# Kernel tuning notes

Measured on AMD Instinct MI355X. Metric: run time of the kernel, lower is better.

The kernel has to match this reference:

```python
import jax, jax.numpy as jnp
import numpy as np

B, F, D = 1024, 4096, 32


def setup_inputs() -> dict:
    key = jax.random.key(0)
    k1, k2, k3, k4 = jax.random.split(key, 4)
    data = jax.random.normal(k1, (B, F), dtype=jnp.float32)
    embed = jax.random.uniform(k2, (F, D), dtype=jnp.float32, minval=-0.05, maxval=0.05)
    bias = jax.random.normal(k3, (F, 1), dtype=jnp.float32) * 0.01
    global_bias = jax.random.normal(k4, (1, 1), dtype=jnp.float32) * 0.01
    return {"data": data, "embed": embed, "bias": bias, "global_bias": global_bias}


def reference(data, embed, bias, global_bias):
    # Original TF: scaled = data[:,:,None] * embed[None]; dot = sum_{i,j} scaled_i . scaled_j
    # Full (diagonal-inclusive) sum of the F x F dot matrix equals ||sum_i scaled_i||^2,
    # identical math in O(B*F*D) instead of O(B*F^2*D).
    scaled = data[:, :, None] * embed[None, :, :]      # (B, F, D)
    s = jnp.sum(scaled, axis=1)                        # (B, D)
    dot = jnp.sum(s * s, axis=-1)                      # (B,)
    bias_term = jnp.sum(data * bias[:, 0][None, :], axis=-1)  # (B,)
    pred = jax.nn.sigmoid(global_bias[0, 0] + bias_term + dot)
    return pred
```

## Files before the change

### kernel.cpp

```cpp
#include <hip/hip_runtime.h>
#include <hip/hip_bf16.h>
#include <math.h>


#define F_DIM 4096
#define D_DIM 32
#define B_DIM 1024
#define MT 16
#define KS 32
#define KC 128
#define LDA 136
#define NW 4

typedef __attribute__((ext_vector_type(8))) short short8;
typedef __attribute__((ext_vector_type(4))) float f32x4;

__device__ inline unsigned int pkbf(float a, float b) {
    __hip_bfloat162 h = __float22bfloat162_rn(make_float2(a, b));
    union { __hip_bfloat162 h2; unsigned int u; } c; c.h2 = h;
    return c.u;
}

__global__ __launch_bounds__(256, 6) void fm_mfma(const float* __restrict__ data,
                                                  const float* __restrict__ embed,
                                                  const float* __restrict__ bias,
                                                  float* __restrict__ ws_s,
                                                  float* __restrict__ ws_b)
{
    __shared__ short lA [MT][LDA];
    __shared__ short lBT[D_DIM][LDA];
    __shared__ float redCT[NW][2][16][20];

    const int t  = threadIdx.x;
    const int w  = t >> 6;
    const int l  = t & 63;
    const int mt = blockIdx.x >> 5;
    const int ks = blockIdx.x & 31;
    const int m0 = mt * MT;
    const int kb = ks * KC;

    const int koff = (l & 31) * 4;
    const float4 bv = *(const float4*)(bias + kb + koff);
    float bt2[2];
    #pragma unroll
    for (int it = 0; it < 2; ++it) {
        const int r = w * 2 + (l >> 5) + it * 8;
        const float4 x = *(const float4*)(data + (size_t)(m0 + r) * F_DIM + kb + koff);
        float s = x.x * bv.x;
        s = fmaf(x.y, bv.y, s);
        s = fmaf(x.z, bv.z, s);
        s = fmaf(x.w, bv.w, s);
        bt2[it] = s;
        uint2 pk;
        pk.x = pkbf(x.x, x.y);
        pk.y = pkbf(x.z, x.w);
        *(uint2*)(&lA[r][koff]) = pk;
    }

    {
        const int d2 = (t & 15) * 2;
        const int k8 = (t >> 4) * 8;
        const float* ep = embed + (size_t)(kb + k8) * D_DIM + d2;
        float2 e[8];
        #pragma unroll
        for (int j = 0; j < 8; ++j) e[j] = *(const float2*)(ep + (size_t)j * D_DIM);
        uint4 ux, uy;
        ux.x = pkbf(e[0].x, e[1].x); ux.y = pkbf(e[2].x, e[3].x);
        ux.z = pkbf(e[4].x, e[5].x); ux.w = pkbf(e[6].x, e[7].x);
        uy.x = pkbf(e[0].y, e[1].y); uy.y = pkbf(e[2].y, e[3].y);
        uy.z = pkbf(e[4].y, e[5].y); uy.w = pkbf(e[6].y, e[7].y);
        *(uint4*)(&lBT[d2    ][k8]) = ux;
        *(uint4*)(&lBT[d2 + 1][k8]) = uy;
    }
    __syncthreads();

    const int quad = l >> 4;
    const int mrow = l & 15;
    const int kk   = w * 32 + quad * 8;
    const short8 a  = *(const short8*)(&lA [mrow     ][kk]);
    const short8 b0 = *(const short8*)(&lBT[mrow     ][kk]);
    const short8 b1 = *(const short8*)(&lBT[16 + mrow][kk]);
    const f32x4 z = {0.f, 0.f, 0.f, 0.f};
    f32x4 acc0 = __builtin_amdgcn_mfma_f32_16x16x32_bf16(a, b0, z, 0, 0, 0);
    f32x4 acc1 = __builtin_amdgcn_mfma_f32_16x16x32_bf16(a, b1, z, 0, 0, 0);

    #pragma unroll
    for (int it = 0; it < 2; ++it) {
        float v = bt2[it];
        v += __shfl_xor(v, 1);  v += __shfl_xor(v, 2);  v += __shfl_xor(v, 4);
        v += __shfl_xor(v, 8);  v += __shfl_xor(v, 16);
        if ((l & 31) == 0)
            ws_b[(size_t)(m0 + w * 2 + (l >> 5) + it * 8) * KS + ks] = v;
    }

    *(f32x4*)(&redCT[w][0][mrow][quad * 4]) = acc0;
    *(f32x4*)(&redCT[w][1][mrow][quad * 4]) = acc1;
    __syncthreads();

    #pragma unroll
    for (int h = 0; h < 2; ++h) {
        const int e  = t + h * 256;
        const int nt = e >> 8;
        const int r  = (e >> 4) & 15;
        const int c  = e & 15;
        const float v = redCT[0][nt][c][r] + redCT[1][nt][c][r]
                      + redCT[2][nt][c][r] + redCT[3][nt][c][r];
        ws_s[((size_t)(m0 + r) * KS + ks) * D_DIM + nt * 16 + c] = v;
    }
}

__global__ __launch_bounds__(256, 4) void fm_final(const float* __restrict__ ws_s,
                                                   const float* __restrict__ ws_b,
                                                   const float* __restrict__ gbias,
                                                   float* __restrict__ out)
{
    const int t = threadIdx.x;
    const int w = t >> 6;
    const int l = t & 63;
    const int row = blockIdx.x * 4 + w;

    float4 v = ((const float4*)(ws_s + (size_t)row * KS * D_DIM))[l];
    #pragma unroll
    for (int m = 8; m <= 32; m <<= 1) {
        v.x += __shfl_xor(v.x, m); v.y += __shfl_xor(v.y, m);
        v.z += __shfl_xor(v.z, m); v.w += __shfl_xor(v.w, m);
    }
    float c = 0.f;
    if (l < 8)  c = v.x * v.x + v.y * v.y + v.z * v.z + v.w * v.w;
    if (l < 32) c += ws_b[(size_t)row * KS + l];
    #pragma unroll
    for (int m = 1; m <= 32; m <<= 1) c += __shfl_xor(c, m);
    if (l == 0) {
        const float x = gbias[0] + c;
        out[row] = 1.0f / (1.0f + __expf(-x));
    }
}

extern "C" void kernel_launch(void* const* d_in, const int* in_sizes, int n_in,
                              void* d_out, int out_size, void* d_ws, size_t ws_size,
                              hipStream_t stream) {
    const float* data  = (const float*)d_in[0];
    const float* embed = (const float*)d_in[1];
    const float* bias  = (const float*)d_in[2];
    const float* gb    = (const float*)d_in[3];
    float* out  = (float*)d_out;

    float* ws_s = (float*)d_ws;
    float* ws_b = (float*)d_ws + (size_t)B_DIM * KS * D_DIM;

    dim3 gridA(64 * KS);
    dim3 blockA(256);
    fm_mfma<<<gridA, blockA, 0, stream>>>(data, embed, bias, ws_s, ws_b);

    dim3 gridB(B_DIM / 4);
    dim3 blockB(256);
    fm_final<<<gridB, blockB, 0, stream>>>(ws_s, ws_b, gb, out);
}
```

Measured before the change: 71.49 us.

## Fuse MFMA partial-sum and final reduction into one cooperative kernel

Merges the two kernels into a single cooperative launch that uses a grid-wide sync between the partial-sum stage and the final sigmoid reduction. The K split drops from 32 to 4 chunks of 1024, and 512-thread blocks accumulate four chained MFMAs per wave. This removes one kernel launch and shrinks the workspace partial traffic. The cost is a grid barrier, only 256 blocks of 512 threads (fewer waves in flight to hide global-load latency), and much larger LDS use per block.

```diff
diff --git a/kernel.cpp b/kernel.cpp
--- a/kernel.cpp
+++ b/kernel.cpp
@@ -1,16 +1,19 @@
 #include <hip/hip_runtime.h>
 #include <hip/hip_bf16.h>
+#include <hip/hip_cooperative_groups.h>
 #include <math.h>
+
+namespace cg = cooperative_groups;
 
 
 #define F_DIM 4096
 #define D_DIM 32
 #define B_DIM 1024
 #define MT 16
-#define KS 32
-#define KC 128
-#define LDA 136
-#define NW 4
+#define KS 4
+#define KC 1024
+#define LDA 1032
+#define NTHREADS 512
 
 typedef __attribute__((ext_vector_type(8))) short short8;
 typedef __attribute__((ext_vector_type(4))) float f32x4;
@@ -21,118 +24,115 @@
     return c.u;
 }
 
-__global__ __launch_bounds__(256, 6) void fm_mfma(const float* __restrict__ data,
-                                                  const float* __restrict__ embed,
-                                                  const float* __restrict__ bias,
-                                                  float* __restrict__ ws_s,
-                                                  float* __restrict__ ws_b)
+__global__ __launch_bounds__(NTHREADS, 2) void fm_fused(
+    const float* __restrict__ data, const float* __restrict__ embed,
+    const float* __restrict__ bias, const float* __restrict__ gbias,
+    float* __restrict__ ws_s, float* __restrict__ ws_b,
+    float* __restrict__ out)
 {
     __shared__ short lA [MT][LDA];
     __shared__ short lBT[D_DIM][LDA];
-    __shared__ float redCT[NW][2][16][20];
+    __shared__ float redCT[8][2][16][20];
 
     const int t  = threadIdx.x;
     const int w  = t >> 6;
     const int l  = t & 63;
-    const int mt = blockIdx.x >> 5;
-    const int ks = blockIdx.x & 31;
+    const int mt = blockIdx.x >> 2;
+    const int ks = blockIdx.x & 3;
     const int m0 = mt * MT;
     const int kb = ks * KC;
 
-    const int koff = (l & 31) * 4;
-    const float4 bv = *(const float4*)(bias + kb + koff);
-    float bt2[2];
-    #pragma unroll
-    for (int it = 0; it < 2; ++it) {
-        const int r = w * 2 + (l >> 5) + it * 8;
-        const float4 x = *(const float4*)(data + (size_t)(m0 + r) * F_DIM + kb + koff);
-        float s = x.x * bv.x;
-        s = fmaf(x.y, bv.y, s);
-        s = fmaf(x.z, bv.z, s);
-        s = fmaf(x.w, bv.w, s);
-        bt2[it] = s;
-        uint2 pk;
-        pk.x = pkbf(x.x, x.y);
-        pk.y = pkbf(x.z, x.w);
-        *(uint2*)(&lA[r][koff]) = pk;
+    {
+        const int r  = t >> 5;
+        const int c4 = (t & 31) * 4;
+        const float* dro = data + (size_t)(m0 + r) * F_DIM + kb;
+        const float* bro = bias + kb;
+        float bt = 0.f;
+        #pragma unroll
+        for (int jj = 0; jj < 8; ++jj) {
+            const int col = c4 + jj * 128;
+            const float4 x  = *(const float4*)(dro + col);
+            const float4 bv = *(const float4*)(bro + col);
+            bt = fmaf(x.x, bv.x, bt);
+            bt = fmaf(x.y, bv.y, bt);
+            bt = fmaf(x.z, bv.z, bt);
+            bt = fmaf(x.w, bv.w, bt);
+            uint2 pk;
+            pk.x = pkbf(x.x, x.y);
+            pk.y = pkbf(x.z, x.w);
+            *(uint2*)(&lA[r][col]) = pk;
+        }
+        bt += __shfl_xor(bt, 1);  bt += __shfl_xor(bt, 2);
+        bt += __shfl_xor(bt, 4);  bt += __shfl_xor(bt, 8);
+        bt += __shfl_xor(bt, 16);
+        if ((t & 31) == 0) ws_b[(size_t)(m0 + r) * KS + ks] = bt;
     }
 
     {
         const int d2 = (t & 15) * 2;
-        const int k8 = (t >> 4) * 8;
-        const float* ep = embed + (size_t)(kb + k8) * D_DIM + d2;
-        float2 e[8];
+        const int kq = t >> 4;
         #pragma unroll
-        for (int j = 0; j < 8; ++j) e[j] = *(const float2*)(ep + (size_t)j * D_DIM);
-        uint4 ux, uy;
-        ux.x = pkbf(e[0].x, e[1].x); ux.y = pkbf(e[2].x, e[3].x);
-        ux.z = pkbf(e[4].x, e[5].x); ux.w = pkbf(e[6].x, e[7].x);
-        uy.x = pkbf(e[0].y, e[1].y); uy.y = pkbf(e[2].y, e[3].y);
-        uy.z = pkbf(e[4].y, e[5].y); uy.w = pkbf(e[6].y, e[7].y);
-        *(uint4*)(&lBT[d2    ][k8]) = ux;
-        *(uint4*)(&lBT[d2 + 1][k8]) = uy;
+        for (int ko = 0; ko < 4; ++ko) {
+            const int k8 = kq * 8 + ko * 256;
+            const float* ep = embed + (size_t)(kb + k8) * D_DIM + d2;
+            float2 e[8];
+            #pragma unroll
+            for (int j = 0; j < 8; ++j) e[j] = *(const float2*)(ep + (size_t)j * D_DIM);
+            uint4 ux, uy;
+            ux.x = pkbf(e[0].x, e[1].x); ux.y = pkbf(e[2].x, e[3].x);
+            ux.z = pkbf(e[4].x, e[5].x); ux.w = pkbf(e[6].x, e[7].x);
+            uy.x = pkbf(e[0].y, e[1].y); uy.y = pkbf(e[2].y, e[3].y);
+            uy.z = pkbf(e[4].y, e[5].y); uy.w = pkbf(e[6].y, e[7].y);
+            *(uint4*)(&lBT[d2    ][k8]) = ux;
+            *(uint4*)(&lBT[d2 + 1][k8]) = uy;
+        }
     }
     __syncthreads();
 
     const int quad = l >> 4;
     const int mrow = l & 15;
-    const int kk   = w * 32 + quad * 8;
-    const short8 a  = *(const short8*)(&lA [mrow     ][kk]);
-    const short8 b0 = *(const short8*)(&lBT[mrow     ][kk]);
-    const short8 b1 = *(const short8*)(&lBT[16 + mrow][kk]);
-    const f32x4 z = {0.f, 0.f, 0.f, 0.f};
-    f32x4 acc0 = __builtin_amdgcn_mfma_f32_16x16x32_bf16(a, b0, z, 0, 0, 0);
-    f32x4 acc1 = __builtin_amdgcn_mfma_f32_16x16x32_bf16(a, b1, z, 0, 0, 0);
-
+    f32x4 acc0 = {0.f, 0.f, 0.f, 0.f};
+    f32x4 acc1 = {0.f, 0.f, 0.f, 0.f};
     #pragma unroll
-    for (int it = 0; it < 2; ++it) {
-        float v = bt2[it];
-        v += __shfl_xor(v, 1);  v += __shfl_xor(v, 2);  v += __shfl_xor(v, 4);
-        v += __shfl_xor(v, 8);  v += __shfl_xor(v, 16);
-        if ((l & 31) == 0)
-            ws_b[(size_t)(m0 + w * 2 + (l >> 5) + it * 8) * KS + ks] = v;
+    for (int s = 0; s < 4; ++s) {
+        const int kk = w * 128 + s * 32 + quad * 8;
+        const short8 a  = *(const short8*)(&lA [mrow     ][kk]);
+        const short8 b0 = *(const short8*)(&lBT[mrow     ][kk]);
+        const short8 b1 = *(const short8*)(&lBT[16 + mrow][kk]);
+        acc0 = __builtin_amdgcn_mfma_f32_16x16x32_bf16(a, b0, acc0, 0, 0, 0);
+        acc1 = __builtin_amdgcn_mfma_f32_16x16x32_bf16(a, b1, acc1, 0, 0, 0);
     }
 
     *(f32x4*)(&redCT[w][0][mrow][quad * 4]) = acc0;
     *(f32x4*)(&redCT[w][1][mrow][quad * 4]) = acc1;
     __syncthreads();
 
-    #pragma unroll
-    for (int h = 0; h < 2; ++h) {
-        const int e  = t + h * 256;
-        const int nt = e >> 8;
-        const int r  = (e >> 4) & 15;
-        const int c  = e & 15;
-        const float v = redCT[0][nt][c][r] + redCT[1][nt][c][r]
-                      + redCT[2][nt][c][r] + redCT[3][nt][c][r];
-        ws_s[((size_t)(m0 + r) * KS + ks) * D_DIM + nt * 16 + c] = v;
+    {
+        const int nt = t >> 8;
+        const int rr = (t >> 4) & 15;
+        const int cc = t & 15;
+        float v = 0.f;
+        #pragma unroll
+        for (int ww = 0; ww < 8; ++ww) v += redCT[ww][nt][cc][rr];
+        ws_s[((size_t)(m0 + rr) * KS + ks) * D_DIM + nt * 16 + cc] = v;
     }
-}
 
-__global__ __launch_bounds__(256, 4) void fm_final(const float* __restrict__ ws_s,
-                                                   const float* __restrict__ ws_b,
-                                                   const float* __restrict__ gbias,
-                                                   float* __restrict__ out)
-{
-    const int t = threadIdx.x;
-    const int w = t >> 6;
-    const int l = t & 63;
-    const int row = blockIdx.x * 4 + w;
+    __threadfence();
+    cg::this_grid().sync();
 
-    float4 v = ((const float4*)(ws_s + (size_t)row * KS * D_DIM))[l];
-    #pragma unroll
-    for (int m = 8; m <= 32; m <<= 1) {
-        v.x += __shfl_xor(v.x, m); v.y += __shfl_xor(v.y, m);
-        v.z += __shfl_xor(v.z, m); v.w += __shfl_xor(v.w, m);
-    }
-    float c = 0.f;
-    if (l < 8)  c = v.x * v.x + v.y * v.y + v.z * v.z + v.w * v.w;
-    if (l < 32) c += ws_b[(size_t)row * KS + l];
-    #pragma unroll
-    for (int m = 1; m <= 32; m <<= 1) c += __shfl_xor(c, m);
-    if (l == 0) {
-        const float x = gbias[0] + c;
-        out[row] = 1.0f / (1.0f + __expf(-x));
+    if (w < 4) {
+        const int row = blockIdx.x * 4 + w;
+        float2 v = ((const float2*)(ws_s + (size_t)row * KS * D_DIM))[l];
+        v.x += __shfl_xor(v.x, 16); v.y += __shfl_xor(v.y, 16);
+        v.x += __shfl_xor(v.x, 32); v.y += __shfl_xor(v.y, 32);
+        float c = (l < 16) ? fmaf(v.x, v.x, v.y * v.y) : 0.f;
+        if (l < 4) c += ws_b[(size_t)row * KS + l];
+        #pragma unroll
+        for (int m = 1; m <= 32; m <<= 1) c += __shfl_xor(c, m);
+        if (l == 0) {
+            const float x = gbias[0] + c;
+            out[row] = 1.0f / (1.0f + __expf(-x));
+        }
     }
 }
 
@@ -148,11 +148,12 @@
     float* ws_s = (float*)d_ws;
     float* ws_b = (float*)d_ws + (size_t)B_DIM * KS * D_DIM;
 
-    dim3 gridA(64 * KS);
-    dim3 blockA(256);
-    fm_mfma<<<gridA, blockA, 0, stream>>>(data, embed, bias, ws_s, ws_b);
+    void* args[7];
+    args[0] = (void*)&data;  args[1] = (void*)&embed; args[2] = (void*)&bias;
+    args[3] = (void*)&gb;    args[4] = (void*)&ws_s;  args[5] = (void*)&ws_b;
+    args[6] = (void*)&out;
 
-    dim3 gridB(B_DIM / 4);
-    dim3 blockB(256);
-    fm_final<<<gridB, blockB, 0, stream>>>(ws_s, ws_b, gb, out);
+    hipLaunchCooperativeKernel((void*)fm_fused,
+                               dim3(B_DIM / MT * KS),
+                               dim3(NTHREADS), args, 0, stream);
 }
```

New measurement: 136.9 us. +91.4%, slower.

## Enlarge M tile, load A directly to registers and fold bias into MFMA

Applied to the files above, without the earlier changes.

Each block now handles 64 rows instead of 16. Each wave owns 16 rows and loops over the full 128-wide K chunk with accumulating MFMAs, which removes the cross-wave LDS reduction and the second barrier. The bias dot product is computed as a third MFMA column tile (bias packed as a bf16 row in LDS) instead of with shuffle reductions, and A is loaded from global straight into registers. The costs are that the bias term is now rounded to bf16, the grid shrinks to a quarter of the blocks, and the stores to ws_s are less coalesced.

```diff
diff --git a/kernel.cpp b/kernel.cpp
--- a/kernel.cpp
+++ b/kernel.cpp
@@ -6,10 +6,10 @@
 #define F_DIM 4096
 #define D_DIM 32
 #define B_DIM 1024
-#define MT 16
+#define MT 64
 #define KS 32
 #define KC 128
-#define LDA 136
+#define LDB 136
 #define NW 4
 
 typedef __attribute__((ext_vector_type(8))) short short8;
@@ -21,15 +21,17 @@
     return c.u;
 }
 
-__global__ __launch_bounds__(256, 6) void fm_mfma(const float* __restrict__ data,
+__device__ inline short8 as_short8(uint4 u) {
+    union { uint4 v; short8 s; } c; c.v = u; return c.s;
+}
+
+__global__ __launch_bounds__(256, 4) void fm_gemm(const float* __restrict__ data,
                                                   const float* __restrict__ embed,
                                                   const float* __restrict__ bias,
                                                   float* __restrict__ ws_s,
                                                   float* __restrict__ ws_b)
 {
-    __shared__ short lA [MT][LDA];
-    __shared__ short lBT[D_DIM][LDA];
-    __shared__ float redCT[NW][2][16][20];
+    __shared__ short lBT[48][LDB];
 
     const int t  = threadIdx.x;
     const int w  = t >> 6;
@@ -38,24 +40,6 @@
     const int ks = blockIdx.x & 31;
     const int m0 = mt * MT;
     const int kb = ks * KC;
-
-    const int koff = (l & 31) * 4;
-    const float4 bv = *(const float4*)(bias + kb + koff);
-    float bt2[2];
-    #pragma unroll
-    for (int it = 0; it < 2; ++it) {
-        const int r = w * 2 + (l >> 5) + it * 8;
-        const float4 x = *(const float4*)(data + (size_t)(m0 + r) * F_DIM + kb + koff);
-        float s = x.x * bv.x;
-        s = fmaf(x.y, bv.y, s);
-        s = fmaf(x.z, bv.z, s);
-        s = fmaf(x.w, bv.w, s);
-        bt2[it] = s;
-        uint2 pk;
-        pk.x = pkbf(x.x, x.y);
-        pk.y = pkbf(x.z, x.w);
-        *(uint2*)(&lA[r][koff]) = pk;
-    }
 
     {
         const int d2 = (t & 15) * 2;
@@ -72,40 +56,51 @@
         *(uint4*)(&lBT[d2    ][k8]) = ux;
         *(uint4*)(&lBT[d2 + 1][k8]) = uy;
     }
+    if (t < 16) {
+        const float4 b0 = *(const float4*)(bias + kb + t * 8);
+        const float4 b1 = *(const float4*)(bias + kb + t * 8 + 4);
+        uint4 u;
+        u.x = pkbf(b0.x, b0.y); u.y = pkbf(b0.z, b0.w);
+        u.z = pkbf(b1.x, b1.y); u.w = pkbf(b1.z, b1.w);
+        *(uint4*)(&lBT[32][t * 8]) = u;
+    }
     __syncthreads();
 
     const int quad = l >> 4;
-    const int mrow = l & 15;
-    const int kk   = w * 32 + quad * 8;
-    const short8 a  = *(const short8*)(&lA [mrow     ][kk]);
-    const short8 b0 = *(const short8*)(&lBT[mrow     ][kk]);
-    const short8 b1 = *(const short8*)(&lBT[16 + mrow][kk]);
-    const f32x4 z = {0.f, 0.f, 0.f, 0.f};
-    f32x4 acc0 = __builtin_amdgcn_mfma_f32_16x16x32_bf16(a, b0, z, 0, 0, 0);
-    f32x4 acc1 = __builtin_amdgcn_mfma_f32_16x16x32_bf16(a, b1, z, 0, 0, 0);
+    const int c    = l & 15;
+    const float* arow = data + (size_t)(m0 + w * 16 + c) * F_DIM + kb;
 
+    f32x4 acc0 = {0.f, 0.f, 0.f, 0.f};
+    f32x4 acc1 = {0.f, 0.f, 0.f, 0.f};
+    f32x4 acc2 = {0.f, 0.f, 0.f, 0.f};
     #pragma unroll
-    for (int it = 0; it < 2; ++it) {
-        float v = bt2[it];
-        v += __shfl_xor(v, 1);  v += __shfl_xor(v, 2);  v += __shfl_xor(v, 4);
-        v += __shfl_xor(v, 8);  v += __shfl_xor(v, 16);
-        if ((l & 31) == 0)
-            ws_b[(size_t)(m0 + w * 2 + (l >> 5) + it * 8) * KS + ks] = v;
+    for (int s = 0; s < 4; ++s) {
+        const int kk = s * 32 + quad * 8;
+        const float4 x0 = *(const float4*)(arow + kk);
+        const float4 x1 = *(const float4*)(arow + kk + 4);
+        uint4 ua;
+        ua.x = pkbf(x0.x, x0.y); ua.y = pkbf(x0.z, x0.w);
+        ua.z = pkbf(x1.x, x1.y); ua.w = pkbf(x1.z, x1.w);
+        const short8 a  = as_short8(ua);
+        const short8 b0 = *(const short8*)(&lBT[c     ][kk]);
+        const short8 b1 = *(const short8*)(&lBT[16 + c][kk]);
+        const short8 b2 = *(const short8*)(&lBT[32 + c][kk]);
+        acc0 = __builtin_amdgcn_mfma_f32_16x16x32_bf16(a, b0, acc0, 0, 0, 0);
+        acc1 = __builtin_amdgcn_mfma_f32_16x16x32_bf16(a, b1, acc1, 0, 0, 0);
+        acc2 = __builtin_amdgcn_mfma_f32_16x16x32_bf16(a, b2, acc2, 0, 0, 0);
     }
 
-    *(f32x4*)(&redCT[w][0][mrow][quad * 4]) = acc0;
-    *(f32x4*)(&redCT[w][1][mrow][quad * 4]) = acc1;
-    __syncthreads();
-
+    const int rbase = m0 + w * 16 + quad * 4;
     #pragma unroll
-    for (int h = 0; h < 2; ++h) {
-        const int e  = t + h * 256;
-        const int nt = e >> 8;
-        const int r  = (e >> 4) & 15;
-        const int c  = e & 15;
-        const float v = redCT[0][nt][c][r] + redCT[1][nt][c][r]
-                      + redCT[2][nt][c][r] + redCT[3][nt][c][r];
-        ws_s[((size_t)(m0 + r) * KS + ks) * D_DIM + nt * 16 + c] = v;
+    for (int j = 0; j < 4; ++j) {
+        float* p = ws_s + ((size_t)(rbase + j) * KS + ks) * D_DIM;
+        p[c]      = acc0[j];
+        p[16 + c] = acc1[j];
+    }
+    if (c == 0) {
+        #pragma unroll
+        for (int j = 0; j < 4; ++j)
+            ws_b[(size_t)(rbase + j) * KS + ks] = acc2[j];
     }
 }
 
@@ -148,9 +143,9 @@
     float* ws_s = (float*)d_ws;
     float* ws_b = (float*)d_ws + (size_t)B_DIM * KS * D_DIM;
 
-    dim3 gridA(64 * KS);
+    dim3 gridA(16 * KS);
     dim3 blockA(256);
-    fm_mfma<<<gridA, blockA, 0, stream>>>(data, embed, bias, ws_s, ws_b);
+    fm_gemm<<<gridA, blockA, 0, stream>>>(data, embed, bias, ws_s, ws_b);
 
     dim3 gridB(B_DIM / 4);
     dim3 blockB(256);
```

Measured after the change: 71.08 us. About the same (-0.6%).
